# Kernel optimization log

Hardware: AMD Instinct MI355X
Metric: run time of the kernel (lower is better)

The kernel has to match this reference:

```python
import jax, jax.numpy as jnp
import numpy as np

B = 524288      # batch
F = 32          # nr_features
C = 10          # nr_classes
H = 64          # hidden_size
D = 2           # tree_depth
NN = 2 ** D - 1 # internal nodes
NL = 2 ** D     # leaf nodes
EPS = 1e-5

# Static tree routing tables, reproducing the original Python int() (truncate-toward-zero) math exactly.
NODE_IDX = np.array([[int((2 ** (d - 1) * (2 ** D + l) - 2 ** D) / 2 ** D) for d in range(D)] for l in range(NL)])  # [NL, D]
PSIGN = np.array([[int(l / 2 ** (D - d)) % 2 for d in range(D)] for l in range(NL)])  # [NL, D]


def _linear_params(key, out_f, in_f):
    k1, k2 = jax.random.split(key)
    bound = 1.0 / np.sqrt(in_f)
    w = jax.random.uniform(k1, (out_f, in_f), minval=-bound, maxval=bound, dtype=jnp.float32)
    b = jax.random.uniform(k2, (out_f,), minval=-bound, maxval=bound, dtype=jnp.float32)
    return w, b


def setup_inputs() -> dict:
    key = jax.random.key(0)
    ks = jax.random.split(key, 6)
    x = jax.random.normal(ks[0], (B, F), dtype=jnp.float32)
    w_in, b_in = _linear_params(ks[1], H, F)
    bn_g = jnp.ones((H,), dtype=jnp.float32)   # BatchNorm1d weight init to 1
    bn_b = jnp.zeros((H,), dtype=jnp.float32)  # BatchNorm1d bias init to 0
    w_fi, b_fi = _linear_params(ks[2], NN * F, H)
    w_fs, b_fs = _linear_params(ks[3], NN * F, H)
    w_lc, b_lc = _linear_params(ks[4], NL * C, H)
    return {"x": x, "w_in": w_in, "b_in": b_in, "bn_g": bn_g, "bn_b": bn_b,
            "w_fi": w_fi, "b_fi": b_fi, "w_fs": w_fs, "b_fs": b_fs,
            "w_lc": w_lc, "b_lc": b_lc}


def reference(x, w_in, b_in, bn_g, bn_b, w_fi, b_fi, w_fs, b_fs, w_lc, b_lc):
    inp = x  # raw features used inside the tree gating
    # input layer + BatchNorm1d (training-mode batch stats, biased var) + exact GELU
    h = x @ w_in.T + b_in                                   # [B, H]
    mu = jnp.mean(h, axis=0)
    var = jnp.var(h, axis=0)
    h = (h - mu) / jnp.sqrt(var + EPS) * bn_g + bn_b
    h = jax.nn.gelu(h, approximate=False)

    fi = (h @ w_fi.T + b_fi).reshape(B, NN, F)              # feature importances per node
    fs = (h @ w_fs.T + b_fs).reshape(B, NN, F)              # feature splits per node
    lc = (h @ w_lc.T + b_lc).reshape(B, NL, C)              # leaf class logits

    smx = jax.nn.softmax(fi, axis=-1)                        # [B, NN, F]
    # node_sd = sigmoid(sum(smx*input) - sum(smx*fs))
    sd = jax.nn.sigmoid(jnp.einsum('bnf,bnf->bn', smx, inp[:, None, :] - fs))  # [B, NN]

    # gate per (leaf, depth): sd if p==0 else 1-sd, at the statically-computed node index
    g = sd[:, NODE_IDX]                                      # [B, NL, D]
    g = jnp.where(PSIGN[None, :, :] == 0, g, 1.0 - g)
    coeff = jnp.prod(g, axis=-1)                             # [B, NL]

    out = jnp.einsum('blc,bl->bc', lc, coeff)                # [B, C]
    return out
```

## Files before the change

### kernel.cpp

```cpp
#include <hip/hip_runtime.h>

typedef __attribute__((ext_vector_type(8))) __bf16 bf16x8;
typedef __attribute__((ext_vector_type(4))) float f32x4;
typedef unsigned short u16;
typedef unsigned int u32;

#define NB 524288
#define EPSI 1e-5f
#define NSHADOW 16

__device__ __forceinline__ float bf2f(u16 h) {
    union { u32 u; float f; } cv; cv.u = ((u32)h) << 16; return cv.f;
}
__device__ __forceinline__ u16 f2bf(float f) {
    __bf16 b = (__bf16)f; return __builtin_bit_cast(u16, b);
}
__device__ __forceinline__ float ldany(const void* p, long i, int isf) {
    return isf ? ((const float*)p)[i] : bf2f(((const u16*)p)[i]);
}

__device__ __forceinline__ float fast_gelu(float v) {
    float t = 1.5957691216057308f * v * (1.0f + 0.044715f * v * v);
    float en = __expf(-t);
    return v * __builtin_amdgcn_rcpf(1.0f + en);
}

template<typename T>
__device__ __forceinline__ void load8f(const T* p, float* o);
template<>
__device__ __forceinline__ void load8f<__bf16>(const __bf16* p, float* o) {
    bf16x8 r = *reinterpret_cast<const bf16x8*>(p);
#pragma unroll
    for (int i = 0; i < 8; ++i) o[i] = (float)r[i];
}
template<>
__device__ __forceinline__ void load8f<float>(const float* p, float* o) {
    f32x4 a = *reinterpret_cast<const f32x4*>(p);
    f32x4 b = *reinterpret_cast<const f32x4*>(p + 4);
#pragma unroll
    for (int i = 0; i < 4; ++i) { o[i] = a[i]; o[4 + i] = b[i]; }
}

__device__ __forceinline__ bf16x8 loadfrag(const __bf16* p) {
    return *reinterpret_cast<const bf16x8*>(p);
}
__device__ __forceinline__ bf16x8 loadfrag(const float* p) {
    f32x4 a = *reinterpret_cast<const f32x4*>(p);
    f32x4 b = *reinterpret_cast<const f32x4*>(p + 4);
    bf16x8 r;
#pragma unroll
    for (int i = 0; i < 4; ++i) { r[i] = (__bf16)a[i]; r[4 + i] = (__bf16)b[i]; }
    return r;
}

__device__ __forceinline__ int detect_isf(const void* x) {
    const int lane = threadIdx.x & 63;
    u32 w0 = ((const u32*)x)[lane];
    u32 w1 = ((const u32*)x)[64 + lane];
    int hit = ((((w0 >> 7) & 0xFFu) >= 0xC0u) || (((w1 >> 7) & 0xFFu) >= 0xC0u)) ? 1 : 0;
    return __ballot(hit) != 0ull;
}

template<int CTRL>
__device__ __forceinline__ float dpp_rot_add(float v) {
    int s = __builtin_amdgcn_update_dpp(0, __builtin_bit_cast(int, v), CTRL, 0xF, 0xF, false);
    return v + __builtin_bit_cast(float, s);
}
__device__ __forceinline__ float row_reduce_add(float v) {
    v = dpp_rot_add<0x121>(v);
    v = dpp_rot_add<0x122>(v);
    v = dpp_rot_add<0x124>(v);
    v = dpp_rot_add<0x128>(v);
    return v;
}

template<typename T>
__device__ __forceinline__ void stats_body(const T* __restrict__ x,
                                           const T* __restrict__ w_in,
                                           float* __restrict__ ws,
                                           float* __restrict__ red) {
    const int lane = threadIdx.x & 63;
    const int wave = threadIdx.x >> 6;
    const int c = lane & 15;
    const int q = lane >> 4;

    bf16x8 b1[4];
#pragma unroll
    for (int nt = 0; nt < 4; ++nt)
        b1[nt] = loadfrag(w_in + (nt * 16 + c) * 32 + q * 8);

    float accs[4][4], accq[4][4];
#pragma unroll
    for (int nt = 0; nt < 4; ++nt)
#pragma unroll
        for (int r = 0; r < 4; ++r) { accs[nt][r] = 0.f; accq[nt][r] = 0.f; }

    const int wid = blockIdx.x * 4 + wave;
    for (int t = 0; t < 4; ++t) {
        const long row0 = ((long)wid * 4 + t) * 16;
        bf16x8 a1 = loadfrag(x + (row0 + c) * 32 + q * 8);
#pragma unroll
        for (int nt = 0; nt < 4; ++nt) {
            f32x4 z = {0.f, 0.f, 0.f, 0.f};
            f32x4 acc = __builtin_amdgcn_mfma_f32_16x16x32_bf16(a1, b1[nt], z, 0, 0, 0);
#pragma unroll
            for (int r = 0; r < 4; ++r) {
                float v = acc[r];
                accs[nt][r] += v;
                accq[nt][r] += v * v;
            }
        }
    }
    for (int i = threadIdx.x; i < 128; i += 256) red[i] = 0.f;
    __syncthreads();
#pragma unroll
    for (int nt = 0; nt < 4; ++nt) {
        float s  = accs[nt][0] + accs[nt][1] + accs[nt][2] + accs[nt][3];
        float sq = accq[nt][0] + accq[nt][1] + accq[nt][2] + accq[nt][3];
        s  += __shfl_xor(s, 16);  s  += __shfl_xor(s, 32);
        sq += __shfl_xor(sq, 16); sq += __shfl_xor(sq, 32);
        if (q == 0) {
            atomicAdd(&red[nt * 16 + c], s);
            atomicAdd(&red[64 + nt * 16 + c], sq);
        }
    }
    __syncthreads();
    float* shard = ws + (blockIdx.x & (NSHADOW - 1)) * 128;
    for (int i = threadIdx.x; i < 128; i += 256) atomicAdd(&shard[i], red[i]);
}

__global__ __launch_bounds__(256) void stats_kernel(
    const void* x, const void* w_in, const void* w_fi, const void* b_fi,
    const void* w_fs, const void* b_fs, const void* w_lc, const void* b_lc,
    float* __restrict__ ws)
{
    const int isf = detect_isf(x);

    if (blockIdx.x < 24) {
        u16* W2p = (u16*)(ws + 2176);
        const int idx = blockIdx.x * 256 + threadIdx.x;
        const int g = idx >> 6, f = idx & 63;
        float v = 0.f;
        if (g < 32)                 v = ldany(w_fi, (long)g * 64 + f, isf);
        else if (g < 64)            v = ldany(w_fs, (long)(g - 32) * 64 + f, isf);
        else if (g < 74)            v = ldany(w_lc, (long)(g - 64) * 64 + f, isf)
                                      + ldany(w_lc, (long)(g - 54) * 64 + f, isf);
        else if (g >= 80 && g < 90) v = ldany(w_lc, (long)(g - 60) * 64 + f, isf)
                                      + ldany(w_lc, (long)(g - 50) * 64 + f, isf);
        W2p[idx] = f2bf(v);
    } else if (blockIdx.x == 24 && threadIdx.x < 96) {
        float* biasP = ws + 2048;
        const int g = threadIdx.x;
        float v = 0.f;
        if (g < 32)                 v = ldany(b_fi, g, isf);
        else if (g < 64)            v = ldany(b_fs, g - 32, isf);
        else if (g < 74)            v = ldany(b_lc, g - 64, isf) + ldany(b_lc, g - 54, isf);
        else if (g >= 80 && g < 90) v = ldany(b_lc, g - 60, isf) + ldany(b_lc, g - 50, isf);
        biasP[g] = v;
    }

    __shared__ float red[128];
    if (isf) stats_body<float>((const float*)x, (const float*)w_in, ws, red);
    else     stats_body<__bf16>((const __bf16*)x, (const __bf16*)w_in, ws, red);
}

template<typename T>
__device__ __forceinline__ void main_body(
    const T* __restrict__ x, const T* __restrict__ bn_g, const T* __restrict__ bn_b,
    const T* __restrict__ w_in, const float* __restrict__ ws, T* __restrict__ out,
    float* __restrict__ sums, float* __restrict__ shs,
    u16* __restrict__ w1s, u16* __restrict__ w2s)
{
    const int tid = threadIdx.x;
    const int lane = tid & 63;
    const int wave = tid >> 6;
    const int c = lane & 15;
    const int q = lane >> 4;
    const float* biasP = ws + 2048;

    if (tid < 128) {
        float s = 0.f;
#pragma unroll
        for (int k = 0; k < NSHADOW; ++k) s += ws[k * 128 + tid];
        sums[tid] = s;
    }
    __syncthreads();

    {
        const int nt = tid >> 6, l = tid & 63, cc = l & 15, qq = l >> 4;
        const int row = 32 * (nt >> 1) + 8 * (cc >> 2) + 4 * (nt & 1) + (cc & 3);
        float mu  = sums[row] * (1.0f / NB);
        float var = fmaxf(sums[64 + row] * (1.0f / NB) - mu * mu, 0.0f);
        float s   = (float)bn_g[row] * rsqrtf(var + EPSI);
        float w8[8];
        load8f(w_in + row * 32 + qq * 8, w8);
        bf16x8 f;
#pragma unroll
        for (int j = 0; j < 8; ++j) f[j] = (__bf16)(w8[j] * s);
        *reinterpret_cast<bf16x8*>(w1s + tid * 8) = f;
    }
    if (tid < 64) {
        const int qq = tid >> 4, nt = (tid >> 2) & 3, r = tid & 3;
        const int ft = 32 * (nt >> 1) + 8 * qq + 4 * (nt & 1) + r;
        float mu  = sums[ft] * (1.0f / NB);
        float var = fmaxf(sums[64 + ft] * (1.0f / NB) - mu * mu, 0.0f);
        float s   = (float)bn_g[ft] * rsqrtf(var + EPSI);
        shs[tid] = (float)bn_b[ft] - mu * s;
    }
    {
        const u32* W2p32 = (const u32*)(ws + 2176);
        for (int k = tid; k < 768; k += 256) {
            const int f = k >> 6, l = k & 63, cc = l & 15, qq = l >> 4;
            const int nt = f >> 1, kt = f & 1;
            const u32* src = W2p32 + ((nt * 16 + cc) * 64 + kt * 32 + qq * 8) / 2;
            u32* dst = (u32*)(w2s + k * 8);
            dst[0] = src[0]; dst[1] = src[1]; dst[2] = src[2]; dst[3] = src[3];
        }
    }
    __syncthreads();

    const float bfi0 = biasP[c],      bfi1 = biasP[16 + c];
    const float bfs0 = biasP[32 + c], bfs1 = biasP[48 + c];
    const float bu   = biasP[64 + c], bv   = biasP[80 + c];

    const long gw = (long)blockIdx.x * 4 + wave;
#pragma unroll 2
    for (int t = 0; t < 2; ++t) {
        u32 tweak = 0;
        asm volatile("" : "+v"(tweak));
        const u16* w1b = w1s + tweak;
        const u16* w2b = w2s + tweak;
        const float* shb = shs + tweak;

        const long row0 = gw * 32 + (long)t * 16;
        bf16x8 a1 = loadfrag(x + (row0 + c) * 32 + q * 8);

        float xv0[4], xv1[4];
#pragma unroll
        for (int r = 0; r < 4; ++r) {
            xv0[r] = (float)x[(row0 + q * 4 + r) * 32 + c];
            xv1[r] = (float)x[(row0 + q * 4 + r) * 32 + 16 + c];
        }

        f32x4 h4[4];
#pragma unroll
        for (int nt = 0; nt < 4; ++nt) {
            bf16x8 b1f = *reinterpret_cast<const bf16x8*>(w1b + (nt * 64 + lane) * 8);
            f32x4 z = {0.f, 0.f, 0.f, 0.f};
            h4[nt] = __builtin_amdgcn_mfma_f32_16x16x32_bf16(b1f, a1, z, 0, 0, 0);
        }

        bf16x8 a2_0, a2_1;
#pragma unroll
        for (int nt = 0; nt < 2; ++nt) {
            f32x4 shA = *reinterpret_cast<const f32x4*>(shb + q * 16 + nt * 4);
            f32x4 shB = *reinterpret_cast<const f32x4*>(shb + q * 16 + (2 + nt) * 4);
#pragma unroll
            for (int r = 0; r < 4; ++r) {
                a2_0[nt * 4 + r] = (__bf16)fast_gelu(h4[nt][r] + shA[r]);
                a2_1[nt * 4 + r] = (__bf16)fast_gelu(h4[2 + nt][r] + shB[r]);
            }
        }

        f32x4 acc[6];
#pragma unroll
        for (int nt = 0; nt < 6; ++nt) {
            bf16x8 f0 = *reinterpret_cast<const bf16x8*>(w2b + ((nt * 2 + 0) * 64 + lane) * 8);
            bf16x8 f1 = *reinterpret_cast<const bf16x8*>(w2b + ((nt * 2 + 1) * 64 + lane) * 8);
            f32x4 z = {0.f, 0.f, 0.f, 0.f};
            acc[nt] = __builtin_amdgcn_mfma_f32_16x16x32_bf16(a2_0, f0, z, 0, 0, 0);
            acc[nt] = __builtin_amdgcn_mfma_f32_16x16x32_bf16(a2_1, f1, acc[nt], 0, 0, 0);
        }

#pragma unroll
        for (int r = 0; r < 4; ++r) {
            float e0  = __expf(acc[0][r] + bfi0);
            float e1  = __expf(acc[1][r] + bfi1);
            float fs0 = acc[2][r] + bfs0;
            float fs1 = acc[3][r] + bfs1;
            float es = row_reduce_add(e0 + e1);
            float dp = row_reduce_add(e0 * (xv0[r] - fs0) + e1 * (xv1[r] - fs1));
            float d  = dp * __builtin_amdgcn_rcpf(es);
            float sd = __builtin_amdgcn_rcpf(1.0f + __expf(-d));
            float uu = acc[4][r] + bu, vv = acc[5][r] + bv;
            float o = sd * (vv + sd * (uu - vv));
            if (c < 10) out[(row0 + q * 4 + r) * 10 + c] = (T)o;
        }
    }
}

__global__ __launch_bounds__(256, 4) void main_kernel(
    const void* x, const void* bn_g, const void* bn_b, const void* w_in,
    float* ws, void* outv)
{
    __shared__ float sums[128];
    __shared__ float shs[64];
    __shared__ __attribute__((aligned(16))) u16 w1s[4 * 64 * 8];
    __shared__ __attribute__((aligned(16))) u16 w2s[12 * 64 * 8];

    if (detect_isf(x))
        main_body<float>((const float*)x, (const float*)bn_g, (const float*)bn_b,
                         (const float*)w_in, ws, (float*)outv, sums, shs, w1s, w2s);
    else
        main_body<__bf16>((const __bf16*)x, (const __bf16*)bn_g, (const __bf16*)bn_b,
                          (const __bf16*)w_in, ws, (__bf16*)outv, sums, shs, w1s, w2s);
}

extern "C" void kernel_launch(void* const* d_in, const int* in_sizes, int n_in,
                              void* d_out, int out_size, void* d_ws, size_t ws_size,
                              hipStream_t stream) {
    float* ws = (float*)d_ws;
    hipMemsetAsync(d_ws, 0, NSHADOW * 128 * sizeof(float), stream);
    stats_kernel<<<2048, 256, 0, stream>>>(d_in[0], d_in[1], d_in[5], d_in[6],
                                           d_in[7], d_in[8], d_in[9], d_in[10], ws);
    main_kernel<<<4096, 256, 0, stream>>>(d_in[0], d_in[3], d_in[4], d_in[1], ws, d_out);
}
```

Baseline: 154.8 us.

## Precompute BN-folded weights once in last stats block; fold biases into MFMA accumulators

The last stats block, detected with an atomic counter, now finalizes the BN statistics once. It writes the BN-scaled first-layer weights, the shift vector, the pre-laid-out second-layer fragments and the biases into a workspace blob. Each main-kernel block then only copies that blob into LDS, instead of every block recomputing the means, variances and scaled weights. Shifts and biases are passed as MFMA accumulator initialisers, and exp is replaced with exp2 by folding log2e into the weights. The x gate values are read with paired vector loads. The finalize step runs serially in one block, and the log2e scaling in bf16 may shift numerics slightly.

```diff
diff --git a/kernel.cpp b/kernel.cpp
--- a/kernel.cpp
+++ b/kernel.cpp
@@ -2,12 +2,15 @@
 
 typedef __attribute__((ext_vector_type(8))) __bf16 bf16x8;
 typedef __attribute__((ext_vector_type(4))) float f32x4;
+typedef __attribute__((ext_vector_type(8))) unsigned short u16x8;
 typedef unsigned short u16;
 typedef unsigned int u32;
 
 #define NB 524288
 #define EPSI 1e-5f
 #define NSHADOW 16
+#define K_LOG2E 1.4426950408889634f
+
 
 __device__ __forceinline__ float bf2f(u16 h) {
     union { u32 u; float f; } cv; cv.u = ((u32)h) << 16; return cv.f;
@@ -19,26 +22,18 @@
     return isf ? ((const float*)p)[i] : bf2f(((const u16*)p)[i]);
 }
 
+#if __has_builtin(__builtin_amdgcn_exp2f)
+#define EXP2F(x) __builtin_amdgcn_exp2f(x)
+#else
+#define EXP2F(x) exp2f(x)
+#endif
+
+#define GK1 2.3022082f
+#define GK2 0.10294324f
 __device__ __forceinline__ float fast_gelu(float v) {
-    float t = 1.5957691216057308f * v * (1.0f + 0.044715f * v * v);
-    float en = __expf(-t);
+    float t2 = v * fmaf(GK2, v * v, GK1);
+    float en = EXP2F(-t2);
     return v * __builtin_amdgcn_rcpf(1.0f + en);
-}
-
-template<typename T>
-__device__ __forceinline__ void load8f(const T* p, float* o);
-template<>
-__device__ __forceinline__ void load8f<__bf16>(const __bf16* p, float* o) {
-    bf16x8 r = *reinterpret_cast<const bf16x8*>(p);
-#pragma unroll
-    for (int i = 0; i < 8; ++i) o[i] = (float)r[i];
-}
-template<>
-__device__ __forceinline__ void load8f<float>(const float* p, float* o) {
-    f32x4 a = *reinterpret_cast<const f32x4*>(p);
-    f32x4 b = *reinterpret_cast<const f32x4*>(p + 4);
-#pragma unroll
-    for (int i = 0; i < 4; ++i) { o[i] = a[i]; o[4 + i] = b[i]; }
 }
 
 __device__ __forceinline__ bf16x8 loadfrag(const __bf16* p) {
@@ -51,6 +46,15 @@
 #pragma unroll
     for (int i = 0; i < 4; ++i) { r[i] = (__bf16)a[i]; r[4 + i] = (__bf16)b[i]; }
     return r;
+}
+
+__device__ __forceinline__ void load2f(const float* p, float& a, float& b) {
+    const float2 v = *reinterpret_cast<const float2*>(p);
+    a = v.x; b = v.y;
+}
+__device__ __forceinline__ void load2f(const __bf16* p, float& a, float& b) {
+    u32 w = *reinterpret_cast<const u32*>(p);
+    a = bf2f((u16)(w & 0xffffu)); b = bf2f((u16)(w >> 16));
 }
 
 __device__ __forceinline__ int detect_isf(const void* x) {
@@ -96,6 +100,7 @@
         for (int r = 0; r < 4; ++r) { accs[nt][r] = 0.f; accq[nt][r] = 0.f; }
 
     const int wid = blockIdx.x * 4 + wave;
+#pragma unroll
     for (int t = 0; t < 4; ++t) {
         const long row0 = ((long)wid * 4 + t) * 16;
         bf16x8 a1 = loadfrag(x + (row0 + c) * 32 + q * 8);
@@ -129,136 +134,161 @@
     for (int i = threadIdx.x; i < 128; i += 256) atomicAdd(&shard[i], red[i]);
 }
 
+__device__ __forceinline__ void finalize_body(
+    const void* w_in, const void* bn_g, const void* bn_b,
+    const void* w_fi, const void* b_fi, const void* w_fs, const void* b_fs,
+    const void* w_lc, const void* b_lc, float* ws, int isf,
+    float* sbuf, float* scl, float* sft)
+{
+    const int tid = threadIdx.x;
+    if (tid < 128) {
+        float s = 0.f;
+#pragma unroll
+        for (int k = 0; k < NSHADOW; ++k)
+            s += __hip_atomic_load(&ws[k * 128 + tid], __ATOMIC_RELAXED, __HIP_MEMORY_SCOPE_AGENT);
+        sbuf[tid] = s;
+    }
+    __syncthreads();
+    if (tid < 64) {
+        float mu  = sbuf[tid] * (1.0f / NB);
+        float var = fmaxf(sbuf[64 + tid] * (1.0f / NB) - mu * mu, 0.0f);
+        float s   = ldany(bn_g, tid, isf) * rsqrtf(var + EPSI);
+        scl[tid] = s;
+        sft[tid] = ldany(bn_b, tid, isf) - mu * s;
+    }
+    __syncthreads();
+    u16* blob = (u16*)((char*)ws + 16384);
+    {
+        const int nt = tid >> 6, l = tid & 63, cc = l & 15, qq = l >> 4;
+        const int row = 32 * (nt >> 1) + 8 * (cc >> 2) + 4 * (nt & 1) + (cc & 3);
+        const float s = scl[row];
+        u16x8 v8;
+#pragma unroll
+        for (int j = 0; j < 8; ++j)
+            v8[j] = f2bf(ldany(w_in, row * 32 + qq * 8 + j, isf) * s);
+        *reinterpret_cast<u16x8*>(blob + tid * 8) = v8;
+    }
+    for (int k = tid; k < 768; k += 256) {
+        const int f = k >> 6, l = k & 63, cc = l & 15, qq = l >> 4;
+        const int nt = f >> 1, kt = f & 1;
+        const int hb = kt * 32 + qq * 8;
+        u16x8 v8;
+        if (nt < 2) {
+            const int ft = 2 * cc + nt;
+#pragma unroll
+            for (int j = 0; j < 8; ++j)
+                v8[j] = f2bf(ldany(w_fi, ft * 64 + hb + j, isf) * K_LOG2E);
+        } else if (nt < 4) {
+            const int ft = 2 * cc + (nt - 2);
+#pragma unroll
+            for (int j = 0; j < 8; ++j)
+                v8[j] = f2bf(ldany(w_fs, ft * 64 + hb + j, isf) * K_LOG2E);
+        } else {
+            const int r0 = ((nt == 4) ? 0 : 20) + cc;
+#pragma unroll
+            for (int j = 0; j < 8; ++j)
+                v8[j] = (cc < 10) ? f2bf(ldany(w_lc, (long)r0 * 64 + hb + j, isf)
+                                       + ldany(w_lc, (long)(r0 + 10) * 64 + hb + j, isf))
+                                  : (u16)0;
+        }
+        *reinterpret_cast<u16x8*>(blob + 2048 + k * 8) = v8;
+    }
+    float* shsp  = (float*)((char*)ws + 16384 + 16384);
+    float* biasp = shsp + 64;
+    if (tid < 64) {
+        const int qq = tid >> 4, nt = (tid >> 2) & 3, r = tid & 3;
+        const int ft = 32 * (nt >> 1) + 8 * qq + 4 * (nt & 1) + r;
+        shsp[tid] = sft[ft];
+    }
+    for (int idx = tid; idx < 384; idx += 256) {
+        const int p = idx >> 2, nt = p >> 4, cc = p & 15;
+        float v = 0.f;
+        if      (nt == 0) v = ldany(b_fi, 2 * cc,     isf) * K_LOG2E;
+        else if (nt == 1) v = ldany(b_fi, 2 * cc + 1, isf) * K_LOG2E;
+        else if (nt == 2) v = ldany(b_fs, 2 * cc,     isf) * K_LOG2E;
+        else if (nt == 3) v = ldany(b_fs, 2 * cc + 1, isf) * K_LOG2E;
+        else if (nt == 4) v = (cc < 10) ? ldany(b_lc, cc,      isf) + ldany(b_lc, 10 + cc, isf) : 0.f;
+        else              v = (cc < 10) ? ldany(b_lc, 20 + cc, isf) + ldany(b_lc, 30 + cc, isf) : 0.f;
+        biasp[idx] = v;
+    }
+    if (tid < 64) biasp[384 + tid] = 0.f;
+}
+
 __global__ __launch_bounds__(256) void stats_kernel(
-    const void* x, const void* w_in, const void* w_fi, const void* b_fi,
-    const void* w_fs, const void* b_fs, const void* w_lc, const void* b_lc,
-    float* __restrict__ ws)
+    const void* x, const void* w_in, const void* bn_g, const void* bn_b,
+    const void* w_fi, const void* b_fi, const void* w_fs, const void* b_fs,
+    const void* w_lc, const void* b_lc, float* __restrict__ ws)
 {
     const int isf = detect_isf(x);
-
-    if (blockIdx.x < 24) {
-        u16* W2p = (u16*)(ws + 2176);
-        const int idx = blockIdx.x * 256 + threadIdx.x;
-        const int g = idx >> 6, f = idx & 63;
-        float v = 0.f;
-        if (g < 32)                 v = ldany(w_fi, (long)g * 64 + f, isf);
-        else if (g < 64)            v = ldany(w_fs, (long)(g - 32) * 64 + f, isf);
-        else if (g < 74)            v = ldany(w_lc, (long)(g - 64) * 64 + f, isf)
-                                      + ldany(w_lc, (long)(g - 54) * 64 + f, isf);
-        else if (g >= 80 && g < 90) v = ldany(w_lc, (long)(g - 60) * 64 + f, isf)
-                                      + ldany(w_lc, (long)(g - 50) * 64 + f, isf);
-        W2p[idx] = f2bf(v);
-    } else if (blockIdx.x == 24 && threadIdx.x < 96) {
-        float* biasP = ws + 2048;
-        const int g = threadIdx.x;
-        float v = 0.f;
-        if (g < 32)                 v = ldany(b_fi, g, isf);
-        else if (g < 64)            v = ldany(b_fs, g - 32, isf);
-        else if (g < 74)            v = ldany(b_lc, g - 64, isf) + ldany(b_lc, g - 54, isf);
-        else if (g >= 80 && g < 90) v = ldany(b_lc, g - 60, isf) + ldany(b_lc, g - 50, isf);
-        biasP[g] = v;
-    }
-
     __shared__ float red[128];
     if (isf) stats_body<float>((const float*)x, (const float*)w_in, ws, red);
     else     stats_body<__bf16>((const __bf16*)x, (const __bf16*)w_in, ws, red);
+
+    __shared__ int lastFlag;
+    __syncthreads();
+    if (threadIdx.x == 0) {
+        __threadfence();
+        u32 prev = atomicAdd((u32*)((char*)ws + 8192), 1u);
+        lastFlag = (prev == (u32)(gridDim.x - 1));
+    }
+    __syncthreads();
+    if (!lastFlag) return;
+    __shared__ float sbuf[128], scl[64], sft[64];
+    finalize_body(w_in, bn_g, bn_b, w_fi, b_fi, w_fs, b_fs, w_lc, b_lc,
+                  ws, isf, sbuf, scl, sft);
 }
 
 template<typename T>
 __device__ __forceinline__ void main_body(
-    const T* __restrict__ x, const T* __restrict__ bn_g, const T* __restrict__ bn_b,
-    const T* __restrict__ w_in, const float* __restrict__ ws, T* __restrict__ out,
-    float* __restrict__ sums, float* __restrict__ shs,
-    u16* __restrict__ w1s, u16* __restrict__ w2s)
+    const T* __restrict__ x, const float* __restrict__ ws, T* __restrict__ out,
+    char* __restrict__ lds)
 {
     const int tid = threadIdx.x;
     const int lane = tid & 63;
     const int wave = tid >> 6;
     const int c = lane & 15;
     const int q = lane >> 4;
-    const float* biasP = ws + 2048;
-
-    if (tid < 128) {
-        float s = 0.f;
-#pragma unroll
-        for (int k = 0; k < NSHADOW; ++k) s += ws[k * 128 + tid];
-        sums[tid] = s;
-    }
-    __syncthreads();
 
     {
-        const int nt = tid >> 6, l = tid & 63, cc = l & 15, qq = l >> 4;
-        const int row = 32 * (nt >> 1) + 8 * (cc >> 2) + 4 * (nt & 1) + (cc & 3);
-        float mu  = sums[row] * (1.0f / NB);
-        float var = fmaxf(sums[64 + row] * (1.0f / NB) - mu * mu, 0.0f);
-        float s   = (float)bn_g[row] * rsqrtf(var + EPSI);
-        float w8[8];
-        load8f(w_in + row * 32 + qq * 8, w8);
-        bf16x8 f;
-#pragma unroll
-        for (int j = 0; j < 8; ++j) f[j] = (__bf16)(w8[j] * s);
-        *reinterpret_cast<bf16x8*>(w1s + tid * 8) = f;
-    }
-    if (tid < 64) {
-        const int qq = tid >> 4, nt = (tid >> 2) & 3, r = tid & 3;
-        const int ft = 32 * (nt >> 1) + 8 * qq + 4 * (nt & 1) + r;
-        float mu  = sums[ft] * (1.0f / NB);
-        float var = fmaxf(sums[64 + ft] * (1.0f / NB) - mu * mu, 0.0f);
-        float s   = (float)bn_g[ft] * rsqrtf(var + EPSI);
-        shs[tid] = (float)bn_b[ft] - mu * s;
-    }
-    {
-        const u32* W2p32 = (const u32*)(ws + 2176);
-        for (int k = tid; k < 768; k += 256) {
-            const int f = k >> 6, l = k & 63, cc = l & 15, qq = l >> 4;
-            const int nt = f >> 1, kt = f & 1;
-            const u32* src = W2p32 + ((nt * 16 + cc) * 64 + kt * 32 + qq * 8) / 2;
-            u32* dst = (u32*)(w2s + k * 8);
-            dst[0] = src[0]; dst[1] = src[1]; dst[2] = src[2]; dst[3] = src[3];
-        }
-    }
-    __syncthreads();
-
-    const float bfi0 = biasP[c],      bfi1 = biasP[16 + c];
-    const float bfs0 = biasP[32 + c], bfs1 = biasP[48 + c];
-    const float bu   = biasP[64 + c], bv   = biasP[80 + c];
+        const f32x4* gsrc = (const f32x4*)((const char*)ws + 16384);
+        f32x4* ldst = (f32x4*)lds;
+        for (int i = tid; i < 1152; i += 256) ldst[i] = gsrc[i];
+    }
+    __syncthreads();
 
     const long gw = (long)blockIdx.x * 4 + wave;
 #pragma unroll 2
     for (int t = 0; t < 2; ++t) {
         u32 tweak = 0;
         asm volatile("" : "+v"(tweak));
-        const u16* w1b = w1s + tweak;
-        const u16* w2b = w2s + tweak;
-        const float* shb = shs + tweak;
+        const u16*   w1b = (const u16*)lds + tweak;
+        const u16*   w2b = (const u16*)(lds + 4096) + tweak;
+        const float* shb = (const float*)(lds + 16384) + tweak;
+        const float* bb  = (const float*)(lds + 16640) + tweak;
 
         const long row0 = gw * 32 + (long)t * 16;
         bf16x8 a1 = loadfrag(x + (row0 + c) * 32 + q * 8);
 
         float xv0[4], xv1[4];
 #pragma unroll
-        for (int r = 0; r < 4; ++r) {
-            xv0[r] = (float)x[(row0 + q * 4 + r) * 32 + c];
-            xv1[r] = (float)x[(row0 + q * 4 + r) * 32 + 16 + c];
-        }
+        for (int r = 0; r < 4; ++r)
+            load2f(x + (row0 + q * 4 + r) * 32 + 2 * c, xv0[r], xv1[r]);
 
         f32x4 h4[4];
 #pragma unroll
         for (int nt = 0; nt < 4; ++nt) {
             bf16x8 b1f = *reinterpret_cast<const bf16x8*>(w1b + (nt * 64 + lane) * 8);
-            f32x4 z = {0.f, 0.f, 0.f, 0.f};
-            h4[nt] = __builtin_amdgcn_mfma_f32_16x16x32_bf16(b1f, a1, z, 0, 0, 0);
+            f32x4 sh = *reinterpret_cast<const f32x4*>(shb + q * 16 + nt * 4);
+            h4[nt] = __builtin_amdgcn_mfma_f32_16x16x32_bf16(b1f, a1, sh, 0, 0, 0);
         }
 
         bf16x8 a2_0, a2_1;
 #pragma unroll
         for (int nt = 0; nt < 2; ++nt) {
-            f32x4 shA = *reinterpret_cast<const f32x4*>(shb + q * 16 + nt * 4);
-            f32x4 shB = *reinterpret_cast<const f32x4*>(shb + q * 16 + (2 + nt) * 4);
 #pragma unroll
             for (int r = 0; r < 4; ++r) {
-                a2_0[nt * 4 + r] = (__bf16)fast_gelu(h4[nt][r] + shA[r]);
-                a2_1[nt * 4 + r] = (__bf16)fast_gelu(h4[2 + nt][r] + shB[r]);
+                a2_0[nt * 4 + r] = (__bf16)fast_gelu(h4[nt][r]);
+                a2_1[nt * 4 + r] = (__bf16)fast_gelu(h4[2 + nt][r]);
             }
         }
 
@@ -267,51 +297,44 @@
         for (int nt = 0; nt < 6; ++nt) {
             bf16x8 f0 = *reinterpret_cast<const bf16x8*>(w2b + ((nt * 2 + 0) * 64 + lane) * 8);
             bf16x8 f1 = *reinterpret_cast<const bf16x8*>(w2b + ((nt * 2 + 1) * 64 + lane) * 8);
-            f32x4 z = {0.f, 0.f, 0.f, 0.f};
-            acc[nt] = __builtin_amdgcn_mfma_f32_16x16x32_bf16(a2_0, f0, z, 0, 0, 0);
+            f32x4 bz = *reinterpret_cast<const f32x4*>(bb + (nt * 16 + c) * 4);
+            acc[nt] = __builtin_amdgcn_mfma_f32_16x16x32_bf16(a2_0, f0, bz, 0, 0, 0);
             acc[nt] = __builtin_amdgcn_mfma_f32_16x16x32_bf16(a2_1, f1, acc[nt], 0, 0, 0);
         }
 
 #pragma unroll
         for (int r = 0; r < 4; ++r) {
-            float e0  = __expf(acc[0][r] + bfi0);
-            float e1  = __expf(acc[1][r] + bfi1);
-            float fs0 = acc[2][r] + bfs0;
-            float fs1 = acc[3][r] + bfs1;
+            float e0 = EXP2F(acc[0][r]);
+            float e1 = EXP2F(acc[1][r]);
+            float t0 = fmaf(K_LOG2E, xv0[r], -acc[2][r]);
+            float t1 = fmaf(K_LOG2E, xv1[r], -acc[3][r]);
             float es = row_reduce_add(e0 + e1);
-            float dp = row_reduce_add(e0 * (xv0[r] - fs0) + e1 * (xv1[r] - fs1));
-            float d  = dp * __builtin_amdgcn_rcpf(es);
-            float sd = __builtin_amdgcn_rcpf(1.0f + __expf(-d));
-            float uu = acc[4][r] + bu, vv = acc[5][r] + bv;
-            float o = sd * (vv + sd * (uu - vv));
+            float dp = row_reduce_add(fmaf(e1, t1, e0 * t0));
+            float d2 = dp * __builtin_amdgcn_rcpf(es);
+            float sd = __builtin_amdgcn_rcpf(1.0f + EXP2F(-d2));
+            float o  = sd * fmaf(sd, acc[4][r] - acc[5][r], acc[5][r]);
             if (c < 10) out[(row0 + q * 4 + r) * 10 + c] = (T)o;
         }
     }
 }
 
 __global__ __launch_bounds__(256, 4) void main_kernel(
-    const void* x, const void* bn_g, const void* bn_b, const void* w_in,
-    float* ws, void* outv)
+    const void* x, const float* __restrict__ ws, void* outv)
 {
-    __shared__ float sums[128];
-    __shared__ float shs[64];
-    __shared__ __attribute__((aligned(16))) u16 w1s[4 * 64 * 8];
-    __shared__ __attribute__((aligned(16))) u16 w2s[12 * 64 * 8];
-
+    __shared__ __attribute__((aligned(16))) char lds[18432];
     if (detect_isf(x))
-        main_body<float>((const float*)x, (const float*)bn_g, (const float*)bn_b,
-                         (const float*)w_in, ws, (float*)outv, sums, shs, w1s, w2s);
+        main_body<float>((const float*)x, ws, (float*)outv, lds);
     else
-        main_body<__bf16>((const __bf16*)x, (const __bf16*)bn_g, (const __bf16*)bn_b,
-                          (const __bf16*)w_in, ws, (__bf16*)outv, sums, shs, w1s, w2s);
+        main_body<__bf16>((const __bf16*)x, ws, (__bf16*)outv, lds);
 }
 
 extern "C" void kernel_launch(void* const* d_in, const int* in_sizes, int n_in,
                               void* d_out, int out_size, void* d_ws, size_t ws_size,
                               hipStream_t stream) {
     float* ws = (float*)d_ws;
-    hipMemsetAsync(d_ws, 0, NSHADOW * 128 * sizeof(float), stream);
-    stats_kernel<<<2048, 256, 0, stream>>>(d_in[0], d_in[1], d_in[5], d_in[6],
-                                           d_in[7], d_in[8], d_in[9], d_in[10], ws);
-    main_kernel<<<4096, 256, 0, stream>>>(d_in[0], d_in[3], d_in[4], d_in[1], ws, d_out);
-}
+    hipMemsetAsync(d_ws, 0, 8448, stream);
+    stats_kernel<<<2048, 256, 0, stream>>>(d_in[0], d_in[1], d_in[3], d_in[4],
+                                           d_in[5], d_in[6], d_in[7], d_in[8],
+                                           d_in[9], d_in[10], ws);
+    main_kernel<<<4096, 256, 0, stream>>>(d_in[0], ws, d_out);
+}
```

Measured after the change: 196.1 us. +26.7%, slower.
